# Optimization experiments

Hardware: AMD Instinct MI355X
Metric: run time of the kernel (lower is better)

## Reference

```python
import jax, jax.numpy as jnp
import numpy as np

Q, C, T, D_IN, D_H = 512, 512, 128, 512, 256


def setup_inputs() -> dict:
    key = jax.random.key(0)
    ks = jax.random.split(key, 8)
    s_in = 1.0 / np.sqrt(D_IN)
    s_h = 1.0 / np.sqrt(D_H)
    return {
        "audio": jax.random.normal(ks[0], (Q, T, D_IN), jnp.float32),
        "video": jax.random.normal(ks[1], (C, T, D_IN), jnp.float32),
        "a_w1": jax.random.normal(ks[2], (D_IN, D_H), jnp.float32) * s_in,
        "a_b1": jnp.zeros((D_H,), jnp.float32),
        "a_w2": jax.random.normal(ks[3], (D_H, D_H), jnp.float32) * s_h,
        "a_b2": jnp.zeros((D_H,), jnp.float32),
        "v_w1": jax.random.normal(ks[4], (D_IN, D_H), jnp.float32) * s_in,
        "v_b1": jnp.zeros((D_H,), jnp.float32),
        "v_w2": jax.random.normal(ks[5], (D_H, D_H), jnp.float32) * s_h,
        "v_b2": jnp.zeros((D_H,), jnp.float32),
        "W": jax.random.normal(ks[6], (D_H, D_H), jnp.float32) * s_h,
        "max_lag": 4,
    }


def _mlp(x, w1, b1, w2, b2):
    # Linear -> ReLU -> Linear
    h = jnp.maximum(x @ w1 + b1, 0.0)
    return h @ w2 + b2


def reference(audio, video, a_w1, a_b1, a_w2, a_b2,
              v_w1, v_b1, v_w2, v_b2, W, max_lag):
    a = _mlp(audio, a_w1, a_b1, a_w2, a_b2)   # [Q, T, D_H]
    v = _mlp(video, v_w1, v_b1, v_w2, v_b2)   # [C, T, D_H]
    # roll along time commutes with the per-frame linear map, so project once
    pv = jnp.einsum('ctd,df->ctf', v, W)      # [C, T, D_H]
    best = None
    for delta in range(-max_lag, max_lag + 1):
        shifted = jnp.roll(pv, delta, axis=1)
        score = jnp.einsum('qtd,ctd->qc', a, shifted)  # [Q, C]
        best = score if best is None else jnp.maximum(best, score)
    return best
```

## Files before the change

### kernel.cpp

```cpp
#include <hip/hip_runtime.h>
#include <cstdint>
#include <cstddef>

typedef __attribute__((ext_vector_type(8))) short frag8;
typedef __attribute__((ext_vector_type(4))) float f32x4;

static __device__ __forceinline__ unsigned short f2bf_r(float f) {
    return (unsigned short)((__float_as_uint(f) + 0x8000u) >> 16);
}

static __device__ __forceinline__ void gll16(const void* g, void* l) {
    __builtin_amdgcn_global_load_lds(
        (const __attribute__((address_space(1))) unsigned int*)g,
        (__attribute__((address_space(3))) unsigned int*)l, 16, 0, 0);
}

__global__ __launch_bounds__(256, 2)
void mlp_fused(const float* __restrict__ X0, const float* __restrict__ X1,
               const unsigned short* __restrict__ W1T0, const unsigned short* __restrict__ W1T1,
               const float* __restrict__ b1v0, const float* __restrict__ b1v1,
               const unsigned short* __restrict__ W2T0, const unsigned short* __restrict__ W2T1,
               const float* __restrict__ b2v0, const float* __restrict__ b2v1,
               unsigned short* __restrict__ O0, unsigned short* __restrict__ O1)
{
    __shared__ __align__(16) unsigned short As[64 * 72];
    __shared__ __align__(16) unsigned short Bs[256 * 64];
    __shared__ __align__(16) unsigned short hs[64 * 264];

    const int mod = blockIdx.y;
    const float* X = mod ? X1 : X0;
    const unsigned short* W1T = mod ? W1T1 : W1T0;
    const unsigned short* W2T = mod ? W2T1 : W2T0;
    const float* b1 = mod ? b1v1 : b1v0;
    const float* b2 = mod ? b2v1 : b2v0;
    unsigned short* O = mod ? O1 : O0;

    const int t    = threadIdx.x;
    const int wave = t >> 6;
    const int lane = t & 63;
    const int quad = lane >> 4;
    const int l15  = lane & 15;
    const int m0   = blockIdx.x * 64;

    const int rowB = lane >> 3;
    const int qB   = (lane & 7) ^ rowB;
    const int nRowBase = wave * 64 + rowB;
    unsigned short* BsW = Bs + wave * 4096;
    const int swz = l15 & 7;

    f32x4 acc[4][4];
    #pragma unroll
    for (int i = 0; i < 4; ++i)
        #pragma unroll
        for (int j = 0; j < 4; ++j)
            acc[i][j] = (f32x4){0.f, 0.f, 0.f, 0.f};

    for (int k0 = 0; k0 < 512; k0 += 64) {
        #pragma unroll
        for (int p = 0; p < 4; ++p) {
            const int idx = p * 256 + t;
            const int row = idx >> 4;
            const int col = (idx & 15) * 4;
            const float4 v = *(const float4*)(X + (size_t)(m0 + row) * 512 + k0 + col);
            const unsigned int a0 = __float_as_uint(v.x) + 0x8000u;
            const unsigned int a1 = __float_as_uint(v.y) + 0x8000u;
            const unsigned int a2 = __float_as_uint(v.z) + 0x8000u;
            const unsigned int a3 = __float_as_uint(v.w) + 0x8000u;
            uint2 pk;
            pk.x = __builtin_amdgcn_perm(a1, a0, 0x07060302u);
            pk.y = __builtin_amdgcn_perm(a3, a2, 0x07060302u);
            *(uint2*)&As[row * 72 + col] = pk;
        }
        #pragma unroll
        for (int p = 0; p < 8; ++p)
            gll16(W1T + (size_t)(nRowBase + p * 8) * 512 + qB * 8 + k0, BsW + p * 512);
        __syncthreads();

        frag8 af[2][4], bf[2][4];
        #pragma unroll
        for (int i = 0; i < 4; ++i)
            #pragma unroll
            for (int kh = 0; kh < 2; ++kh)
                af[kh][i] = *(const frag8*)&As[(i * 16 + l15) * 72 + kh * 32 + quad * 8];
        #pragma unroll
        for (int j = 0; j < 4; ++j) {
            const int row = wave * 64 + j * 16 + l15;
            #pragma unroll
            for (int kh = 0; kh < 2; ++kh)
                bf[kh][j] = *(const frag8*)&Bs[row * 64 + (((kh * 4 + quad) ^ swz) * 8)];
        }
        #pragma unroll
        for (int kh = 0; kh < 2; ++kh)
            #pragma unroll
            for (int i = 0; i < 4; ++i)
                #pragma unroll
                for (int j = 0; j < 4; ++j)
                    acc[i][j] = __builtin_amdgcn_mfma_f32_16x16x32_bf16(af[kh][i], bf[kh][j], acc[i][j], 0, 0, 0);
        __syncthreads();
    }

    #pragma unroll
    for (int j = 0; j < 4; ++j) {
        const int col = wave * 64 + j * 16 + l15;
        const float bv = b1[col];
        #pragma unroll
        for (int i = 0; i < 4; ++i) {
            const int rl = i * 16 + quad * 4;
            #pragma unroll
            for (int r = 0; r < 4; ++r)
                hs[(rl + r) * 264 + col] = f2bf_r(fmaxf(acc[i][j][r] + bv, 0.0f));
        }
    }
    __syncthreads();

    #pragma unroll
    for (int i = 0; i < 4; ++i)
        #pragma unroll
        for (int j = 0; j < 4; ++j)
            acc[i][j] = (f32x4){0.f, 0.f, 0.f, 0.f};

    for (int k0 = 0; k0 < 256; k0 += 64) {
        #pragma unroll
        for (int p = 0; p < 8; ++p)
            gll16(W2T + (size_t)(nRowBase + p * 8) * 256 + qB * 8 + k0, BsW + p * 512);
        __syncthreads();

        frag8 af[2][4], bf[2][4];
        #pragma unroll
        for (int i = 0; i < 4; ++i)
            #pragma unroll
            for (int kh = 0; kh < 2; ++kh)
                af[kh][i] = *(const frag8*)&hs[(i * 16 + l15) * 264 + k0 + kh * 32 + quad * 8];
        #pragma unroll
        for (int j = 0; j < 4; ++j) {
            const int row = wave * 64 + j * 16 + l15;
            #pragma unroll
            for (int kh = 0; kh < 2; ++kh)
                bf[kh][j] = *(const frag8*)&Bs[row * 64 + (((kh * 4 + quad) ^ swz) * 8)];
        }
        #pragma unroll
        for (int kh = 0; kh < 2; ++kh)
            #pragma unroll
            for (int i = 0; i < 4; ++i)
                #pragma unroll
                for (int j = 0; j < 4; ++j)
                    acc[i][j] = __builtin_amdgcn_mfma_f32_16x16x32_bf16(af[kh][i], bf[kh][j], acc[i][j], 0, 0, 0);
        __syncthreads();
    }

    #pragma unroll
    for (int j = 0; j < 4; ++j) {
        const int col = wave * 64 + j * 16 + l15;
        const float bv = b2[col];
        #pragma unroll
        for (int i = 0; i < 4; ++i) {
            const int rl = i * 16 + quad * 4;
            #pragma unroll
            for (int r = 0; r < 4; ++r)
                hs[(rl + r) * 264 + col] = f2bf_r(acc[i][j][r] + bv);
        }
    }
    __syncthreads();
    #pragma unroll
    for (int u = 0; u < 8; ++u) {
        const int chunk = u * 256 + t;
        const int row = chunk >> 5;
        const int c16 = (chunk & 31) * 8;
        uint4 v = *(const uint4*)&hs[row * 264 + c16];
        *(uint4*)&O[(size_t)(m0 + row) * 256 + c16] = v;
    }
}

__global__ __launch_bounds__(512, 2)
void gemm_corr(const unsigned short* __restrict__ A, const unsigned short* __restrict__ B,
               float* __restrict__ partial, int sc)
{
    __shared__ __align__(16) unsigned short lds[4 * 2 * 8192];

    const int t    = threadIdx.x;
    const int wave = t >> 6;
    const int lane = t & 63;
    const int quad = lane >> 4;
    const int l15  = lane & 15;
    const int wr   = wave >> 2;
    const int wc   = wave & 3;

    const int L = blockIdx.x + (blockIdx.y << 1) + (blockIdx.z << 2);
    int ell;
    if (sc == 7) {
        const int xcd = L & 7, off = L >> 3;
        ell = (xcd < 4 ? xcd * 32 : 128 + (xcd - 4) * 31) + off;
    } else {
        const int xcd = L & 7, off = L >> 3;
        ell = xcd * 18 + off;
    }
    const int bx   = ell & 1;
    const int by   = (ell >> 1) & 1;
    const int rest = ell >> 2;
    const int d    = rest % 9;
    const int s    = rest / 9;
    const int m0   = by * 256;
    const int n0   = bx * 256;

    int t0, nT;
    if (sc == 7) { nT = (s == 6) ? 136 : 148; t0 = s * 148; }
    else         { nT = 256;                  t0 = s << 8; }
    const int zp     = d * sc + s;
    const int delta  = d - 4;
    const int kStart = t0 * 32;
    const int koff   = (32768 - 256 * delta) & 32767;

    const int gsrc      = (lane & 7) ^ ((lane >> 3) & 7);
    const int srcRowOff = ((lane >> 3) << 1) + (gsrc >> 2);
    const int srcCol    = (gsrc & 3) << 3;
    const size_t aSrcBase = (size_t)(m0 + srcRowOff) * 32768 + srcCol;
    const size_t bSrcBase = (size_t)(n0 + srcRowOff) * 32768 + srcCol;

    const int gphys = (((l15 & 1) << 2) | quad) ^ ((l15 >> 1) & 7);
    const int aOff  = (wr * 64 + (l15 >> 1)) * 64 + gphys * 8;
    const int bOff  = (wc * 32 + (l15 >> 1)) * 64 + gphys * 8;

    f32x4 acc[8][4];
    #pragma unroll
    for (int i = 0; i < 8; ++i)
        #pragma unroll
        for (int j = 0; j < 4; ++j)
            acc[i][j] = (f32x4){0.f, 0.f, 0.f, 0.f};

    frag8 bfb[2][4];

    #pragma unroll
    for (int pt = 0; pt < 3; ++pt) {
        const int kk = (kStart + pt * 32) & 32767;
        const int kb = (kk + koff) & 32767;
        #pragma unroll
        for (int qq = 0; qq < 2; ++qq) {
            const int c = wave * 2 + qq;
            gll16(A + aSrcBase + (size_t)c * 16 * 32768 + kk, &lds[pt * 16384 + c * 512]);
            gll16(B + bSrcBase + (size_t)c * 16 * 32768 + kb, &lds[pt * 16384 + 8192 + c * 512]);
        }
    }
    asm volatile("s_waitcnt vmcnt(8)" ::: "memory");
    __builtin_amdgcn_s_barrier();
    asm volatile("" ::: "memory");
    #pragma unroll
    for (int j = 0; j < 4; ++j)
        bfb[0][j] = *(const frag8*)(&lds[8192] + bOff + j * 512);

    for (int kt0 = 0; kt0 < nT; kt0 += 4) {
        #pragma unroll
        for (int u = 0; u < 4; ++u) {
            {
                const int kk = (kStart + (kt0 + u + 3) * 32) & 32767;
                const int kb = (kk + koff) & 32767;
                unsigned short* LSa = &lds[((u + 3) & 3) * 16384 + wave * 1024];
                unsigned short* LSb = LSa + 8192;
                #pragma unroll
                for (int qq = 0; qq < 2; ++qq) {
                    const int c = wave * 2 + qq;
                    gll16(A + aSrcBase + (size_t)c * 16 * 32768 + kk, LSa + qq * 512);
                    gll16(B + bSrcBase + (size_t)c * 16 * 32768 + kb, LSb + qq * 512);
                }
            }
            asm volatile("s_waitcnt vmcnt(8)" ::: "memory");
            __builtin_amdgcn_s_barrier();
            asm volatile("" ::: "memory");

            const unsigned short* LA  = &lds[u * 16384];
            const unsigned short* LBn = &lds[((u + 1) & 3) * 16384 + 8192];
            frag8 af[8];
            #pragma unroll
            for (int i = 0; i < 4; ++i) af[i] = *(const frag8*)(LA + aOff + i * 512);
            __builtin_amdgcn_s_setprio(1);
            #pragma unroll
            for (int i = 0; i < 4; ++i)
                #pragma unroll
                for (int j = 0; j < 4; ++j)
                    acc[i][j] = __builtin_amdgcn_mfma_f32_16x16x32_bf16(af[i], bfb[u & 1][j], acc[i][j], 0, 0, 0);
            __builtin_amdgcn_s_setprio(0);
            #pragma unroll
            for (int i = 4; i < 8; ++i) af[i] = *(const frag8*)(LA + aOff + i * 512);
            #pragma unroll
            for (int j = 0; j < 4; ++j)
                bfb[(u + 1) & 1][j] = *(const frag8*)(LBn + bOff + j * 512);
            __builtin_amdgcn_s_setprio(1);
            #pragma unroll
            for (int i = 4; i < 8; ++i)
                #pragma unroll
                for (int j = 0; j < 4; ++j)
                    acc[i][j] = __builtin_amdgcn_mfma_f32_16x16x32_bf16(af[i], bfb[u & 1][j], acc[i][j], 0, 0, 0);
            __builtin_amdgcn_s_setprio(0);
            asm volatile("" ::: "memory");
            __builtin_amdgcn_s_barrier();
        }
    }
    asm volatile("s_waitcnt vmcnt(0)" ::: "memory");

    float* C = partial + ((size_t)zp << 18);
    #pragma unroll
    for (int i = 0; i < 8; ++i) {
        const int rg = m0 + wr * 128 + i * 16 + quad * 4;
        #pragma unroll
        for (int j = 0; j < 4; ++j) {
            const int cg = n0 + wc * 64 + j * 16 + l15;
            #pragma unroll
            for (int r = 0; r < 4; ++r)
                C[(size_t)(rg + r) * 512 + cg] = acc[i][j][r];
        }
    }
}

__global__ void prep(const float* __restrict__ a_w1, const float* __restrict__ v_w1,
                     const float* __restrict__ a_w2, const float* __restrict__ v_w2,
                     const float* __restrict__ W, const float* __restrict__ v_b2,
                     unsigned short* __restrict__ aw1T, unsigned short* __restrict__ vw1T,
                     unsigned short* __restrict__ aw2T,
                     unsigned short* __restrict__ WcT, float* __restrict__ bc)
{
    const int b = blockIdx.x;
    __shared__ float tl[32][33];
    __shared__ float wcol[256];
    if (b < 320) {
        const float* src; unsigned short* dst; int R, C, tile;
        if (b < 128)      { src = a_w1; dst = aw1T; R = 512; C = 256; tile = b; }
        else if (b < 256) { src = v_w1; dst = vw1T; R = 512; C = 256; tile = b - 128; }
        else              { src = a_w2; dst = aw2T; R = 256; C = 256; tile = b - 256; }
        const int tilesX = C / 32;
        const int bx = (tile % tilesX) * 32, by = (tile / tilesX) * 32;
        const int tx = threadIdx.x & 31, ty = threadIdx.x >> 5;
        #pragma unroll
        for (int r = ty; r < 32; r += 8)
            tl[r][tx] = src[(size_t)(by + r) * C + bx + tx];
        __syncthreads();
        #pragma unroll
        for (int c = ty; c < 32; c += 8)
            dst[(size_t)(bx + c) * R + by + tx] = f2bf_r(tl[tx][c]);
    } else {
        const int n = b - 320, k = threadIdx.x;
        wcol[k] = W[(size_t)k * 256 + n];
        __syncthreads();
        float s = 0.f;
        #pragma unroll 8
        for (int d = 0; d < 256; ++d) s += v_w2[(size_t)k * 256 + d] * wcol[d];
        WcT[(size_t)n * 256 + k] = f2bf_r(s);
        if (k == 0) {
            float tt = 0.f;
            for (int d = 0; d < 256; ++d) tt += v_b2[d] * wcol[d];
            bc[n] = tt;
        }
    }
}

__global__ void reduce_max(const float* __restrict__ partial, float* __restrict__ out, int sc) {
    const int idx = blockIdx.x * blockDim.x + threadIdx.x;
    float best = -3.4e38f;
    for (int d = 0; d < 9; ++d) {
        float ssum = 0.f;
        const float* p = partial + ((size_t)(d * sc) << 18) + idx;
        for (int k = 0; k < sc; ++k) ssum += p[(size_t)k << 18];
        best = fmaxf(best, ssum);
    }
    out[idx] = best;
}

extern "C" void kernel_launch(void* const* d_in, const int* in_sizes, int n_in,
                              void* d_out, int out_size, void* d_ws, size_t ws_size,
                              hipStream_t stream) {
    const float* audio = (const float*)d_in[0];
    const float* video = (const float*)d_in[1];
    const float* a_w1  = (const float*)d_in[2];
    const float* a_b1  = (const float*)d_in[3];
    const float* a_w2  = (const float*)d_in[4];
    const float* a_b2  = (const float*)d_in[5];
    const float* v_w1  = (const float*)d_in[6];
    const float* v_b1  = (const float*)d_in[7];
    const float* v_w2  = (const float*)d_in[8];
    const float* v_b2  = (const float*)d_in[9];
    const float* Wm    = (const float*)d_in[10];

    char* ws = (char*)d_ws;
    unsigned short* aw1T = (unsigned short*)(ws + 0);
    unsigned short* vw1T = (unsigned short*)(ws + 262144);
    unsigned short* aw2T = (unsigned short*)(ws + 524288);
    unsigned short* WcT  = (unsigned short*)(ws + 655360);
    float*          bc   = (float*)(ws + 786432);
    unsigned short* a_bf = (unsigned short*)(ws + 1048576);
    unsigned short* pv   = (unsigned short*)(ws + 34603008);
    float* partial       = (float*)(ws + 68157440);
    float* out = (float*)d_out;

    const int sc = (ws_size >= 134217728ull) ? 7 : 4;

    prep<<<dim3(576), 256, 0, stream>>>(a_w1, v_w1, a_w2, v_w2, Wm, v_b2,
                                        aw1T, vw1T, aw2T, WcT, bc);
    mlp_fused<<<dim3(1024, 2), 256, 0, stream>>>(
        audio, video, aw1T, vw1T, a_b1, v_b1, aw2T, WcT, a_b2, bc, a_bf, pv);
    gemm_corr<<<dim3(2, 2, 9 * sc), 512, 0, stream>>>(a_bf, pv, partial, sc);
    reduce_max<<<dim3(1024), 256, 0, stream>>>(partial, out, sc);
}
```

Measured before the change: 485.3 us.

## Double-buffer and prefetch MLP GEMM stages with 128-row tiles and 512 threads

The fused MLP kernel now handles 128 rows per block with 8 waves in a 2x4 layout, which halves the number of times weight tiles are loaded per row. Weights are staged into two LDS slots and the next fp32 input tile is loaded into registers ahead of use, so global loads overlap MFMA work. Raw s_barrier calls with explicit waitcnt replace __syncthreads, and setprio is raised around the MFMA bursts. LDS is aliased between the input tile and the hidden buffer to fit. The trade-offs are higher register pressure, fewer blocks per CU, and fragile manual vmcnt accounting.

```diff
diff --git a/kernel.cpp b/kernel.cpp
--- a/kernel.cpp
+++ b/kernel.cpp
@@ -15,7 +15,7 @@
         (__attribute__((address_space(3))) unsigned int*)l, 16, 0, 0);
 }
 
-__global__ __launch_bounds__(256, 2)
+__global__ __launch_bounds__(512, 2)
 void mlp_fused(const float* __restrict__ X0, const float* __restrict__ X1,
                const unsigned short* __restrict__ W1T0, const unsigned short* __restrict__ W1T1,
                const float* __restrict__ b1v0, const float* __restrict__ b1v1,
@@ -23,9 +23,10 @@
                const float* __restrict__ b2v0, const float* __restrict__ b2v1,
                unsigned short* __restrict__ O0, unsigned short* __restrict__ O1)
 {
-    __shared__ __align__(16) unsigned short As[64 * 72];
-    __shared__ __align__(16) unsigned short Bs[256 * 64];
-    __shared__ __align__(16) unsigned short hs[64 * 264];
+    __shared__ __align__(16) unsigned short smem[33792 + 32768];
+    unsigned short* hs = smem;
+    unsigned short* As = smem;
+    unsigned short* Bs = smem + 33792;
 
     const int mod = blockIdx.y;
     const float* X = mod ? X1 : X0;
@@ -40,13 +41,15 @@
     const int lane = t & 63;
     const int quad = lane >> 4;
     const int l15  = lane & 15;
-    const int m0   = blockIdx.x * 64;
+    const int wr   = wave >> 2;
+    const int wc   = wave & 3;
+    const int m0   = blockIdx.x * 128;
 
     const int rowB = lane >> 3;
     const int qB   = (lane & 7) ^ rowB;
-    const int nRowBase = wave * 64 + rowB;
-    unsigned short* BsW = Bs + wave * 4096;
-    const int swz = l15 & 7;
+    const int swz  = l15 & 7;
+    const int aRow = t >> 4;
+    const int aCol = (t & 15) * 4;
 
     f32x4 acc[4][4];
     #pragma unroll
@@ -55,106 +58,166 @@
         for (int j = 0; j < 4; ++j)
             acc[i][j] = (f32x4){0.f, 0.f, 0.f, 0.f};
 
-    for (int k0 = 0; k0 < 512; k0 += 64) {
-        #pragma unroll
-        for (int p = 0; p < 4; ++p) {
-            const int idx = p * 256 + t;
-            const int row = idx >> 4;
-            const int col = (idx & 15) * 4;
-            const float4 v = *(const float4*)(X + (size_t)(m0 + row) * 512 + k0 + col);
-            const unsigned int a0 = __float_as_uint(v.x) + 0x8000u;
-            const unsigned int a1 = __float_as_uint(v.y) + 0x8000u;
-            const unsigned int a2 = __float_as_uint(v.z) + 0x8000u;
-            const unsigned int a3 = __float_as_uint(v.w) + 0x8000u;
-            uint2 pk;
-            pk.x = __builtin_amdgcn_perm(a1, a0, 0x07060302u);
-            pk.y = __builtin_amdgcn_perm(a3, a2, 0x07060302u);
-            *(uint2*)&As[row * 72 + col] = pk;
-        }
-        #pragma unroll
-        for (int p = 0; p < 8; ++p)
-            gll16(W1T + (size_t)(nRowBase + p * 8) * 512 + qB * 8 + k0, BsW + p * 512);
-        __syncthreads();
-
-        frag8 af[2][4], bf[2][4];
-        #pragma unroll
-        for (int i = 0; i < 4; ++i)
-            #pragma unroll
-            for (int kh = 0; kh < 2; ++kh)
-                af[kh][i] = *(const frag8*)&As[(i * 16 + l15) * 72 + kh * 32 + quad * 8];
-        #pragma unroll
-        for (int j = 0; j < 4; ++j) {
-            const int row = wave * 64 + j * 16 + l15;
-            #pragma unroll
-            for (int kh = 0; kh < 2; ++kh)
-                bf[kh][j] = *(const frag8*)&Bs[row * 64 + (((kh * 4 + quad) ^ swz) * 8)];
-        }
-        #pragma unroll
-        for (int kh = 0; kh < 2; ++kh)
-            #pragma unroll
-            for (int i = 0; i < 4; ++i)
-                #pragma unroll
-                for (int j = 0; j < 4; ++j)
-                    acc[i][j] = __builtin_amdgcn_mfma_f32_16x16x32_bf16(af[kh][i], bf[kh][j], acc[i][j], 0, 0, 0);
-        __syncthreads();
+#define MLP_CONV(XR)                                                              \
+    _Pragma("unroll")                                                             \
+    for (int p = 0; p < 4; ++p) {                                                 \
+        const float4 v = XR[p];                                                   \
+        const unsigned int a0 = __float_as_uint(v.x) + 0x8000u;                   \
+        const unsigned int a1 = __float_as_uint(v.y) + 0x8000u;                   \
+        const unsigned int a2 = __float_as_uint(v.z) + 0x8000u;                   \
+        const unsigned int a3 = __float_as_uint(v.w) + 0x8000u;                   \
+        uint2 pk;                                                                 \
+        pk.x = __builtin_amdgcn_perm(a1, a0, 0x07060302u);                        \
+        pk.y = __builtin_amdgcn_perm(a3, a2, 0x07060302u);                        \
+        *(uint2*)&As[(p * 32 + aRow) * 72 + aCol] = pk;                           \
+    }
+
+#define MLP_XLOAD(XR, K0)                                                         \
+    _Pragma("unroll")                                                             \
+    for (int p = 0; p < 4; ++p)                                                   \
+        XR[p] = *(const float4*)(X + (size_t)(m0 + p * 32 + aRow) * 512 + (K0) + aCol);
+
+#define MLP_STAGE_W(WT, STRIDE, K0, SLOT)                                         \
+    _Pragma("unroll")                                                             \
+    for (int p = 0; p < 4; ++p)                                                   \
+        gll16(WT + (size_t)(p * 64 + wave * 8 + rowB) * (STRIDE) + qB * 8 + (K0), \
+              Bs + (SLOT) * 16384 + p * 4096 + wave * 512);
+
+#define MLP_COMPUTE(SLOT)                                                         \
+    {                                                                             \
+        frag8 af_[2][4], bf_[2][4];                                               \
+        _Pragma("unroll")                                                         \
+        for (int i = 0; i < 4; ++i)                                               \
+            _Pragma("unroll")                                                     \
+            for (int kh = 0; kh < 2; ++kh)                                        \
+                af_[kh][i] = *(const frag8*)&As[(wr * 64 + i * 16 + l15) * 72 + kh * 32 + quad * 8]; \
+        _Pragma("unroll")                                                         \
+        for (int j = 0; j < 4; ++j) {                                             \
+            const int row_ = wc * 64 + j * 16 + l15;                              \
+            _Pragma("unroll")                                                     \
+            for (int kh = 0; kh < 2; ++kh)                                        \
+                bf_[kh][j] = *(const frag8*)&Bs[(SLOT) * 16384 + row_ * 64 + (((kh * 4 + quad) ^ swz) * 8)]; \
+        }                                                                         \
+        __builtin_amdgcn_s_setprio(1);                                            \
+        _Pragma("unroll")                                                         \
+        for (int kh = 0; kh < 2; ++kh)                                            \
+            _Pragma("unroll")                                                     \
+            for (int i = 0; i < 4; ++i)                                           \
+                _Pragma("unroll")                                                 \
+                for (int j = 0; j < 4; ++j)                                       \
+                    acc[i][j] = __builtin_amdgcn_mfma_f32_16x16x32_bf16(af_[kh][i], bf_[kh][j], acc[i][j], 0, 0, 0); \
+        __builtin_amdgcn_s_setprio(0);                                            \
+    }
+
+    float4 xrA[4], xrB[4];
+    MLP_XLOAD(xrA, 0)
+    MLP_STAGE_W(W1T, 512, 0, 0)
+
+    for (int kk = 0; kk < 8; kk += 2) {
+        {
+            const int k0 = kk * 64;
+            MLP_CONV(xrA)
+            MLP_XLOAD(xrB, k0 + 64)
+            MLP_STAGE_W(W1T, 512, k0 + 64, 1)
+            asm volatile("s_waitcnt lgkmcnt(0)" ::: "memory");
+            asm volatile("s_waitcnt vmcnt(8)" ::: "memory");
+            __builtin_amdgcn_s_barrier();
+            asm volatile("" ::: "memory");
+            MLP_COMPUTE(0)
+            asm volatile("" ::: "memory");
+            __builtin_amdgcn_s_barrier();
+            asm volatile("" ::: "memory");
+        }
+        {
+            const int k0 = (kk + 1) * 64;
+            MLP_CONV(xrB)
+            if (kk < 6) {
+                MLP_XLOAD(xrA, k0 + 64)
+                MLP_STAGE_W(W1T, 512, k0 + 64, 0)
+                asm volatile("s_waitcnt lgkmcnt(0)" ::: "memory");
+                asm volatile("s_waitcnt vmcnt(8)" ::: "memory");
+            } else {
+                MLP_STAGE_W(W2T, 256, 0, 0)
+                asm volatile("s_waitcnt lgkmcnt(0)" ::: "memory");
+                asm volatile("s_waitcnt vmcnt(4)" ::: "memory");
+            }
+            __builtin_amdgcn_s_barrier();
+            asm volatile("" ::: "memory");
+            MLP_COMPUTE(1)
+            asm volatile("" ::: "memory");
+            __builtin_amdgcn_s_barrier();
+            asm volatile("" ::: "memory");
+        }
     }
 
     #pragma unroll
     for (int j = 0; j < 4; ++j) {
-        const int col = wave * 64 + j * 16 + l15;
+        const int col = wc * 64 + j * 16 + l15;
         const float bv = b1[col];
         #pragma unroll
         for (int i = 0; i < 4; ++i) {
-            const int rl = i * 16 + quad * 4;
+            const int rl = wr * 64 + i * 16 + quad * 4;
             #pragma unroll
             for (int r = 0; r < 4; ++r)
                 hs[(rl + r) * 264 + col] = f2bf_r(fmaxf(acc[i][j][r] + bv, 0.0f));
         }
     }
-    __syncthreads();
-
     #pragma unroll
     for (int i = 0; i < 4; ++i)
         #pragma unroll
         for (int j = 0; j < 4; ++j)
             acc[i][j] = (f32x4){0.f, 0.f, 0.f, 0.f};
-
-    for (int k0 = 0; k0 < 256; k0 += 64) {
-        #pragma unroll
-        for (int p = 0; p < 8; ++p)
-            gll16(W2T + (size_t)(nRowBase + p * 8) * 256 + qB * 8 + k0, BsW + p * 512);
-        __syncthreads();
-
-        frag8 af[2][4], bf[2][4];
-        #pragma unroll
-        for (int i = 0; i < 4; ++i)
+    asm volatile("s_waitcnt lgkmcnt(0)" ::: "memory");
+    __builtin_amdgcn_s_barrier();
+    asm volatile("" ::: "memory");
+
+    #pragma unroll
+    for (int k = 0; k < 4; ++k) {
+        const int k0 = k * 64;
+        if (k < 3) {
+            MLP_STAGE_W(W2T, 256, k0 + 64, (k + 1) & 1)
+            asm volatile("s_waitcnt vmcnt(4)" ::: "memory");
+        } else {
+            asm volatile("s_waitcnt vmcnt(0)" ::: "memory");
+        }
+        __builtin_amdgcn_s_barrier();
+        asm volatile("" ::: "memory");
+        {
+            frag8 af_[2][4], bf_[2][4];
+            #pragma unroll
+            for (int i = 0; i < 4; ++i)
+                #pragma unroll
+                for (int kh = 0; kh < 2; ++kh)
+                    af_[kh][i] = *(const frag8*)&hs[(wr * 64 + i * 16 + l15) * 264 + k0 + kh * 32 + quad * 8];
+            #pragma unroll
+            for (int j = 0; j < 4; ++j) {
+                const int row_ = wc * 64 + j * 16 + l15;
+                #pragma unroll
+                for (int kh = 0; kh < 2; ++kh)
+                    bf_[kh][j] = *(const frag8*)&Bs[((k & 1) * 16384) + row_ * 64 + (((kh * 4 + quad) ^ swz) * 8)];
+            }
+            __builtin_amdgcn_s_setprio(1);
             #pragma unroll
             for (int kh = 0; kh < 2; ++kh)
-                af[kh][i] = *(const frag8*)&hs[(i * 16 + l15) * 264 + k0 + kh * 32 + quad * 8];
-        #pragma unroll
-        for (int j = 0; j < 4; ++j) {
-            const int row = wave * 64 + j * 16 + l15;
-            #pragma unroll
-            for (int kh = 0; kh < 2; ++kh)
-                bf[kh][j] = *(const frag8*)&Bs[row * 64 + (((kh * 4 + quad) ^ swz) * 8)];
-        }
-        #pragma unroll
-        for (int kh = 0; kh < 2; ++kh)
-            #pragma unroll
-            for (int i = 0; i < 4; ++i)
-                #pragma unroll
-                for (int j = 0; j < 4; ++j)
-                    acc[i][j] = __builtin_amdgcn_mfma_f32_16x16x32_bf16(af[kh][i], bf[kh][j], acc[i][j], 0, 0, 0);
-        __syncthreads();
+                #pragma unroll
+                for (int i = 0; i < 4; ++i)
+                    #pragma unroll
+                    for (int j = 0; j < 4; ++j)
+                        acc[i][j] = __builtin_amdgcn_mfma_f32_16x16x32_bf16(af_[kh][i], bf_[kh][j], acc[i][j], 0, 0, 0);
+            __builtin_amdgcn_s_setprio(0);
+        }
+        asm volatile("" ::: "memory");
+        __builtin_amdgcn_s_barrier();
+        asm volatile("" ::: "memory");
     }
 
     #pragma unroll
     for (int j = 0; j < 4; ++j) {
-        const int col = wave * 64 + j * 16 + l15;
+        const int col = wc * 64 + j * 16 + l15;
         const float bv = b2[col];
         #pragma unroll
         for (int i = 0; i < 4; ++i) {
-            const int rl = i * 16 + quad * 4;
+            const int rl = wr * 64 + i * 16 + quad * 4;
             #pragma unroll
             for (int r = 0; r < 4; ++r)
                 hs[(rl + r) * 264 + col] = f2bf_r(acc[i][j][r] + bv);
@@ -163,12 +226,16 @@
     __syncthreads();
     #pragma unroll
     for (int u = 0; u < 8; ++u) {
-        const int chunk = u * 256 + t;
+        const int chunk = u * 512 + t;
         const int row = chunk >> 5;
         const int c16 = (chunk & 31) * 8;
         uint4 v = *(const uint4*)&hs[row * 264 + c16];
         *(uint4*)&O[(size_t)(m0 + row) * 256 + c16] = v;
     }
+#undef MLP_CONV
+#undef MLP_XLOAD
+#undef MLP_STAGE_W
+#undef MLP_COMPUTE
 }
 
 __global__ __launch_bounds__(512, 2)
@@ -393,7 +460,7 @@
 
     prep<<<dim3(576), 256, 0, stream>>>(a_w1, v_w1, a_w2, v_w2, Wm, v_b2,
                                         aw1T, vw1T, aw2T, WcT, bc);
-    mlp_fused<<<dim3(1024, 2), 256, 0, stream>>>(
+    mlp_fused<<<dim3(512, 2), 512, 0, stream>>>(
         audio, video, aw1T, vw1T, a_b1, v_b1, aw2T, WcT, a_b2, bc, a_bf, pv);
     gemm_corr<<<dim3(2, 2, 9 * sc), 512, 0, stream>>>(a_bf, pv, partial, sc);
     reduce_max<<<dim3(1024), 256, 0, stream>>>(partial, out, sc);
```

New measurement: 499.0 us. 1.03x slower.

## Switch correlation GEMM to 32x32x16 bf16 MFMA tiles

Applied to the files above, without the earlier changes.

Rewrites the inner loop of the correlation GEMM to use 32x32x16 MFMA instructions on 32x32 output tiles instead of 16x16x32 on 16x16 tiles. This cuts the number of LDS fragment loads per MFMA, since each wave's 128x64 tile is now 4x2 blocks. It also drops the cross-stage B-fragment prefetch and loosens the vmcnt wait from 8 to 12. Fragment addressing, swizzle and the output store mapping are rebuilt to match the new layout. Loads are no longer overlapped with compute inside a stage, so exposed LDS latency could increase.

```diff
diff --git a/kernel.cpp b/kernel.cpp
--- a/kernel.cpp
+++ b/kernel.cpp
@@ -4,6 +4,7 @@
 
 typedef __attribute__((ext_vector_type(8))) short frag8;
 typedef __attribute__((ext_vector_type(4))) float f32x4;
+typedef __attribute__((ext_vector_type(16))) float f32x16;
 
 static __device__ __forceinline__ unsigned short f2bf_r(float f) {
     return (unsigned short)((__float_as_uint(f) + 0x8000u) >> 16);
@@ -180,8 +181,6 @@
     const int t    = threadIdx.x;
     const int wave = t >> 6;
     const int lane = t & 63;
-    const int quad = lane >> 4;
-    const int l15  = lane & 15;
     const int wr   = wave >> 2;
     const int wc   = wave & 3;
 
@@ -216,18 +215,23 @@
     const size_t aSrcBase = (size_t)(m0 + srcRowOff) * 32768 + srcCol;
     const size_t bSrcBase = (size_t)(n0 + srcRowOff) * 32768 + srcCol;
 
-    const int gphys = (((l15 & 1) << 2) | quad) ^ ((l15 >> 1) & 7);
-    const int aOff  = (wr * 64 + (l15 >> 1)) * 64 + gphys * 8;
-    const int bOff  = (wc * 32 + (l15 >> 1)) * 64 + gphys * 8;
-
-    f32x4 acc[8][4];
-    #pragma unroll
-    for (int i = 0; i < 8; ++i)
-        #pragma unroll
-        for (int j = 0; j < 4; ++j)
-            acc[i][j] = (f32x4){0.f, 0.f, 0.f, 0.f};
-
-    frag8 bfb[2][4];
+    const int rpA  = (lane >> 1) & 15;
+    const int oct  = lane >> 5;
+    const int par  = lane & 1;
+    const int swz7 = (lane >> 1) & 7;
+    int gph[2];
+    #pragma unroll
+    for (int kh = 0; kh < 2; ++kh)
+        gph[kh] = (((par << 2) | (kh << 1) | oct) ^ swz7) * 8;
+
+    f32x16 acc[4][2];
+    #pragma unroll
+    for (int i = 0; i < 4; ++i)
+        #pragma unroll
+        for (int j = 0; j < 2; ++j)
+            #pragma unroll
+            for (int r = 0; r < 16; ++r)
+                acc[i][j][r] = 0.f;
 
     #pragma unroll
     for (int pt = 0; pt < 3; ++pt) {
@@ -240,12 +244,6 @@
             gll16(B + bSrcBase + (size_t)c * 16 * 32768 + kb, &lds[pt * 16384 + 8192 + c * 512]);
         }
     }
-    asm volatile("s_waitcnt vmcnt(8)" ::: "memory");
-    __builtin_amdgcn_s_barrier();
-    asm volatile("" ::: "memory");
-    #pragma unroll
-    for (int j = 0; j < 4; ++j)
-        bfb[0][j] = *(const frag8*)(&lds[8192] + bOff + j * 512);
 
     for (int kt0 = 0; kt0 < nT; kt0 += 4) {
         #pragma unroll
@@ -262,33 +260,31 @@
                     gll16(B + bSrcBase + (size_t)c * 16 * 32768 + kb, LSb + qq * 512);
                 }
             }
-            asm volatile("s_waitcnt vmcnt(8)" ::: "memory");
+            asm volatile("s_waitcnt vmcnt(12)" ::: "memory");
             __builtin_amdgcn_s_barrier();
             asm volatile("" ::: "memory");
 
-            const unsigned short* LA  = &lds[u * 16384];
-            const unsigned short* LBn = &lds[((u + 1) & 3) * 16384 + 8192];
-            frag8 af[8];
-            #pragma unroll
-            for (int i = 0; i < 4; ++i) af[i] = *(const frag8*)(LA + aOff + i * 512);
+            const unsigned short* LA = &lds[u * 16384];
+            const unsigned short* LB = LA + 8192;
+            frag8 af[4][2], bf[2][2];
+            #pragma unroll
+            for (int j = 0; j < 2; ++j)
+                #pragma unroll
+                for (int kh = 0; kh < 2; ++kh)
+                    bf[j][kh] = *(const frag8*)(LB + (wc * 32 + j * 16 + rpA) * 64 + gph[kh]);
+            #pragma unroll
+            for (int i = 0; i < 4; ++i)
+                #pragma unroll
+                for (int kh = 0; kh < 2; ++kh)
+                    af[i][kh] = *(const frag8*)(LA + (wr * 64 + i * 16 + rpA) * 64 + gph[kh]);
             __builtin_amdgcn_s_setprio(1);
             #pragma unroll
-            for (int i = 0; i < 4; ++i)
-                #pragma unroll
-                for (int j = 0; j < 4; ++j)
-                    acc[i][j] = __builtin_amdgcn_mfma_f32_16x16x32_bf16(af[i], bfb[u & 1][j], acc[i][j], 0, 0, 0);
-            __builtin_amdgcn_s_setprio(0);
-            #pragma unroll
-            for (int i = 4; i < 8; ++i) af[i] = *(const frag8*)(LA + aOff + i * 512);
-            #pragma unroll
-            for (int j = 0; j < 4; ++j)
-                bfb[(u + 1) & 1][j] = *(const frag8*)(LBn + bOff + j * 512);
-            __builtin_amdgcn_s_setprio(1);
-            #pragma unroll
-            for (int i = 4; i < 8; ++i)
-                #pragma unroll
-                for (int j = 0; j < 4; ++j)
-                    acc[i][j] = __builtin_amdgcn_mfma_f32_16x16x32_bf16(af[i], bfb[u & 1][j], acc[i][j], 0, 0, 0);
+            for (int kh = 0; kh < 2; ++kh)
+                #pragma unroll
+                for (int i = 0; i < 4; ++i)
+                    #pragma unroll
+                    for (int j = 0; j < 2; ++j)
+                        acc[i][j] = __builtin_amdgcn_mfma_f32_32x32x16_bf16(af[i][kh], bf[j][kh], acc[i][j], 0, 0, 0);
             __builtin_amdgcn_s_setprio(0);
             asm volatile("" ::: "memory");
             __builtin_amdgcn_s_barrier();
@@ -297,15 +293,18 @@
     asm volatile("s_waitcnt vmcnt(0)" ::: "memory");
 
     float* C = partial + ((size_t)zp << 18);
-    #pragma unroll
-    for (int i = 0; i < 8; ++i) {
-        const int rg = m0 + wr * 128 + i * 16 + quad * 4;
-        #pragma unroll
-        for (int j = 0; j < 4; ++j) {
-            const int cg = n0 + wc * 64 + j * 16 + l15;
-            #pragma unroll
-            for (int r = 0; r < 4; ++r)
-                C[(size_t)(rg + r) * 512 + cg] = acc[i][j][r];
+    const int cgl = lane & 31;
+    #pragma unroll
+    for (int i = 0; i < 4; ++i) {
+        const int rgBase = m0 + wr * 128 + i * 32 + 4 * oct;
+        #pragma unroll
+        for (int j = 0; j < 2; ++j) {
+            const int cg = n0 + wc * 64 + j * 32 + cgl;
+            #pragma unroll
+            for (int rq = 0; rq < 4; ++rq)
+                #pragma unroll
+                for (int r = 0; r < 4; ++r)
+                    C[(size_t)(rgBase + rq * 8 + r) * 512 + cg] = acc[i][j][rq * 4 + r];
         }
     }
 }
```

New measurement: 501.4 us. 1.03x slower.
